# Kernel tuning notes

Measured on AMD Instinct MI355X. Metric: run time of the kernel, lower is better.

Reference implementation:

```python
import jax, jax.numpy as jnp
import numpy as np

# ---- model hyperparameters (match init_kwargs) ----
D_MODEL = 1024
D_STATE = 128
EXPAND = 2
HEADDIM = 64
NGROUPS = 1
D_INNER = EXPAND * D_MODEL            # 2048
NHEADS = D_INNER // HEADDIM           # 32
ROPE_FRAC = 0.5
SPLIT = int(D_STATE * ROPE_FRAC)      # 64 rotary dims
NANG = SPLIT // 2                     # 32 rope angles
A_FLOOR = 1e-4
EPS = 1e-5
BATCH, SEQLEN = 1, 1024
SIZES = [D_INNER, D_INNER, D_STATE * NGROUPS, D_STATE * NGROUPS, NHEADS, NHEADS, NHEADS, NANG]
D_IN_PROJ = int(np.sum(SIZES))        # 4480


def setup_inputs() -> dict:
    key = jax.random.key(0)
    ks = jax.random.split(key, 6)
    u = jax.random.normal(ks[0], (BATCH, SEQLEN, D_MODEL), dtype=jnp.float32)
    W_in = jax.random.normal(ks[1], (D_MODEL, D_IN_PROJ), dtype=jnp.float32) * 0.02
    # dt_bias ~ log(dt) for dt in [1e-3, 0.1] -> around -4
    dt_bias = jax.random.normal(ks[2], (NHEADS,), dtype=jnp.float32) * 0.5 - 4.0
    B_bias = jnp.ones((NHEADS, D_STATE), jnp.float32) + 0.01 * jax.random.normal(ks[3], (NHEADS, D_STATE), dtype=jnp.float32)
    C_bias = jnp.ones((NHEADS, D_STATE), jnp.float32) + 0.01 * jax.random.normal(ks[4], (NHEADS, D_STATE), dtype=jnp.float32)
    Bn_w = jnp.ones((D_STATE,), jnp.float32)
    Cn_w = jnp.ones((D_STATE,), jnp.float32)
    D_param = jnp.ones((NHEADS,), jnp.float32)
    W_out = jax.random.normal(ks[5], (D_INNER, D_MODEL), dtype=jnp.float32) * 0.02
    return {"u": u, "W_in": W_in, "dt_bias": dt_bias, "B_bias": B_bias, "C_bias": C_bias,
            "Bn_w": Bn_w, "Cn_w": Cn_w, "D_param": D_param, "W_out": W_out}


def _rmsnorm(v, w):
    return v * jax.lax.rsqrt(jnp.mean(v * v, axis=-1, keepdims=True) + EPS) * w


def _forward(u, W_in, dt_bias, B_bias, C_bias, Bn_w, Cn_w, D_param, W_out):
    b, l, _ = u.shape
    proj = u @ W_in                                   # (b, l, d_in_proj)
    idx = np.cumsum(SIZES)[:-1]
    z, x, Bp, Cp, dd_dt, dd_A, trap_raw, ang = jnp.split(proj, idx, axis=-1)
    z = z.reshape(b, l, NHEADS, HEADDIM)
    x = x.reshape(b, l, NHEADS, HEADDIM)
    # A = clamp(-softplus(.), max=-A_floor);  dt = softplus(. + dt_bias)
    A = jnp.minimum(-jax.nn.softplus(dd_A), -A_FLOOR)          # (b,l,H)
    dt = jax.nn.softplus(dd_dt + dt_bias)                      # (b,l,H)
    a = jnp.exp(A * dt)                                        # decay per step
    lam = jax.nn.sigmoid(trap_raw)                             # trapezoid gate
    # RMSNorm on B/C (ngroups=1), then per-head additive bias
    Bn = _rmsnorm(Bp, Bn_w)                                    # (b,l,N)
    Cn = _rmsnorm(Cp, Cn_w)
    Bh = Bn[:, :, None, :] + B_bias                            # (b,l,H,N)
    Ch = Cn[:, :, None, :] + C_bias
    # data-dependent rotary: cumulative angle = cumsum(angles * dt)
    theta = jnp.cumsum(ang[:, :, None, :] * dt[..., None], axis=1)  # (b,l,H,NANG)
    cos, sin = jnp.cos(theta), jnp.sin(theta)

    def rope(v):
        d1, d2, rest = v[..., :NANG], v[..., NANG:SPLIT], v[..., SPLIT:]
        return jnp.concatenate([d1 * cos - d2 * sin, d1 * sin + d2 * cos, rest], axis=-1)

    Bh, Ch = rope(Bh), rope(Ch)

    tfirst = lambda v: jnp.moveaxis(v, 1, 0)
    inputs = (tfirst(Bh), tfirst(Ch), tfirst(x), tfirst(a), tfirst(dt), tfirst(lam))
    h0 = jnp.zeros((b, NHEADS, HEADDIM, D_STATE), jnp.float32)
    k0 = jnp.zeros((b, NHEADS, D_STATE), jnp.float32)
    v0 = jnp.zeros((b, NHEADS, HEADDIM), jnp.float32)

    def step(carry, inp):
        h, kp, vp = carry
        Bt, Ct, xt, at, dtt, lamt = inp
        # trapezoidal selective-scan update:
        # h_t = a_t h_{t-1} + dt_t (lam_t B_t x_t + (1-lam_t) a_t B_{t-1} x_{t-1})
        cur = jnp.einsum('bhp,bhn->bhpn', xt, Bt) * (dtt * lamt)[..., None, None]
        prv = jnp.einsum('bhp,bhn->bhpn', vp, kp) * (dtt * (1.0 - lamt) * at)[..., None, None]
        h = at[..., None, None] * h + cur + prv
        yt = jnp.einsum('bhn,bhpn->bhp', Ct, h)
        return (h, Bt, xt), yt

    _, y = jax.lax.scan(step, (h0, k0, v0), inputs)          # (l,b,H,P)
    y = jnp.moveaxis(y, 0, 1) + D_param[None, None, :, None] * x
    y = y * jax.nn.silu(z)                                    # gated output (no out-proj norm)
    return y.reshape(b, l, D_INNER) @ W_out


def reference(u, W_in, dt_bias, B_bias, C_bias, Bn_w, Cn_w, D_param, W_out):
    return _forward(u, W_in, dt_bias, B_bias, C_bias, Bn_w, Cn_w, D_param, W_out)
```

## Files before the change

### kernel.cpp

```cpp
#include <hip/hip_runtime.h>
#include <stdint.h>

#define SEQ     1024

typedef __attribute__((ext_vector_type(8))) short short8;
typedef __attribute__((ext_vector_type(4))) float f4;

__device__ __forceinline__ short f2b(float f){
  union { float f; uint32_t u; } v; v.f = f;
  uint32_t r = (v.u + 0x7fffu + ((v.u >> 16) & 1u)) >> 16;
  return (short)(uint16_t)r;
}
__device__ __forceinline__ float b2f(uint16_t u){
  union { uint32_t u; float f; } v; v.u = ((uint32_t)u) << 16; return v.f;
}
__device__ __forceinline__ uint32_t pack2(float lo, float hi){
  return (uint32_t)(uint16_t)f2b(lo) | ((uint32_t)(uint16_t)f2b(hi) << 16);
}
__device__ __forceinline__ float softplus_f(float x){
  return x > 20.f ? x : log1pf(__expf(x));
}
__device__ __forceinline__ void gload_lds16(const short* g, short* l){
  __builtin_amdgcn_global_load_lds((const __attribute__((address_space(1))) void*)g,
                                   (__attribute__((address_space(3))) void*)l, 16, 0, 0);
}

__global__ __launch_bounds__(256) void prep_inputs(const float* __restrict__ u, short* __restrict__ u16,
                                                   const float* __restrict__ W_in, short* __restrict__ WtIn,
                                                   const float* __restrict__ W_out, short* __restrict__ WtOut,
                                                   float* __restrict__ outz){
  int b = blockIdx.x;
  int tid = threadIdx.x;
  if (b < 1024){
    int i = (b * 256 + tid) * 4;
    f4 v = *(const f4*)(u + i);
    uint2 pk; pk.x = pack2(v.x, v.y); pk.y = pack2(v.z, v.w);
    *(uint2*)(u16 + i) = pk;
    return;
  }
  if (b >= 2656){
    int i = ((b - 2656) * 256 + tid) * 4;
    *(f4*)(outz + i) = (f4){0.f, 0.f, 0.f, 0.f};
    return;
  }
  const float* in; short* outp; int R, lda, bx, by;
  if (b < 2144){ int idx = b - 1024; bx = idx % 140; by = idx / 140; in = W_in;  outp = WtIn;  R = 1024; lda = 4480; }
  else         { int idx = b - 2144; bx = idx & 31;  by = idx >> 5;  in = W_out; outp = WtOut; R = 2048; lda = 1024; }
  __shared__ float tile[32][132];
  int bc = bx * 32, br = by * 128;
  int c = tid & 31, r0 = tid >> 5;
  #pragma unroll
  for (int i = 0; i < 16; i++){
    int r = r0 + i * 8;
    tile[c][r] = in[(size_t)(br + r) * lda + bc + c];
  }
  __syncthreads();
  #pragma unroll
  for (int i = 0; i < 4; i++){
    int task = tid + 256 * i;
    int cc = task >> 5;
    int rg = (task & 31) * 4;
    f4 v = *(const f4*)&tile[cc][rg];
    uint2 pk; pk.x = pack2(v.x, v.y); pk.y = pack2(v.z, v.w);
    *(uint2*)(outp + (size_t)(bc + cc) * R + br + rg) = pk;
  }
}

__global__ __launch_bounds__(256) void gemm1_kernel(const short* __restrict__ A, const short* __restrict__ Bt,
                                                    short* __restrict__ zx, short* __restrict__ xTb,
                                                    float* __restrict__ projT){
  const int K = 1024;
  __shared__ __align__(16) short As[2][128 * 32];
  __shared__ __align__(16) short Bs[2][160 * 32];
  const int tid  = threadIdx.x;
  const int wave = tid >> 6;
  const int lane = tid & 63;
  const int m0 = blockIdx.y * 128;
  const int n0 = blockIdx.x * 160;
  const int wm = (wave >> 1) * 64;
  const int wn = (wave & 1) * 80;
  const int quad = lane >> 4;
  const int r16  = lane & 15;

  f4 acc[4][5];
  #pragma unroll
  for (int i = 0; i < 4; i++)
    #pragma unroll
    for (int j = 0; j < 5; j++) acc[i][j] = (f4){0.f, 0.f, 0.f, 0.f};

  const int row0 = tid >> 2;
  const int kq   = tid & 3;
  const short* gA0 = A  + (size_t)(m0 + row0) * K + kq * 8;
  const short* gA1 = A  + (size_t)(m0 + row0 + 64) * K + kq * 8;
  const short* gB0 = Bt + (size_t)(n0 + row0) * K + kq * 8;
  const short* gB1 = Bt + (size_t)(n0 + row0 + 64) * K + kq * 8;
  const short* gB2 = Bt + (size_t)(n0 + row0 + 128) * K + kq * 8;

  gload_lds16(gA0, &As[0][(size_t)tid * 8]);
  gload_lds16(gA1, &As[0][(size_t)(tid + 256) * 8]);
  gload_lds16(gB0, &Bs[0][(size_t)tid * 8]);
  gload_lds16(gB1, &Bs[0][(size_t)(tid + 256) * 8]);
  if (tid < 128) gload_lds16(gB2, &Bs[0][(size_t)(tid + 512) * 8]);

  for (int kt = 0; kt < 32; ++kt){
    const int cur = kt & 1;
    __syncthreads();
    if (kt + 1 < 32){
      const int ko = (kt + 1) * 32;
      const int nxt = cur ^ 1;
      gload_lds16(gA0 + ko, &As[nxt][(size_t)tid * 8]);
      gload_lds16(gA1 + ko, &As[nxt][(size_t)(tid + 256) * 8]);
      gload_lds16(gB0 + ko, &Bs[nxt][(size_t)tid * 8]);
      gload_lds16(gB1 + ko, &Bs[nxt][(size_t)(tid + 256) * 8]);
      if (tid < 128) gload_lds16(gB2 + ko, &Bs[nxt][(size_t)(tid + 512) * 8]);
    }
    short8 af[4], bf[5];
    #pragma unroll
    for (int i = 0; i < 4; i++)
      af[i] = *(const short8*)&As[cur][(wm + i * 16 + r16) * 32 + quad * 8];
    #pragma unroll
    for (int j = 0; j < 5; j++)
      bf[j] = *(const short8*)&Bs[cur][(wn + j * 16 + r16) * 32 + quad * 8];
    #pragma unroll
    for (int i = 0; i < 4; i++)
      #pragma unroll
      for (int j = 0; j < 5; j++)
        acc[i][j] = __builtin_amdgcn_mfma_f32_16x16x32_bf16(af[i], bf[j], acc[i][j], 0, 0, 0);
  }

  #pragma unroll
  for (int i = 0; i < 4; i++)
    #pragma unroll
    for (int j = 0; j < 5; j++){
      int colb = n0 + wn + j * 16 + r16;
      int rowb = m0 + wm + i * 16 + quad * 4;
      if (colb < 2048){
        #pragma unroll
        for (int rr = 0; rr < 4; ++rr)
          zx[(size_t)(rowb + rr) * 4096 + colb] = f2b(acc[i][j][rr]);
      } else if (colb < 4096){
        uint2 pk; pk.x = pack2(acc[i][j][0], acc[i][j][1]); pk.y = pack2(acc[i][j][2], acc[i][j][3]);
        *(uint2*)(xTb + (size_t)(colb - 2048) * 1024 + rowb) = pk;
        #pragma unroll
        for (int rr = 0; rr < 4; ++rr)
          zx[(size_t)(rowb + rr) * 4096 + colb] = f2b(acc[i][j][rr]);
      } else {
        #pragma unroll
        for (int rr = 0; rr < 4; ++rr)
          projT[(size_t)(rowb + rr) * 384 + (colb - 4096)] = acc[i][j][rr];
      }
    }
}

__global__ __launch_bounds__(256) void gemm2_kernel(const short* __restrict__ A, const short* __restrict__ Bt,
                                                    float* __restrict__ C){
  const int N = 1024, K = 2048, klen = 512;
  __shared__ __align__(16) short As[2][128 * 32];
  __shared__ __align__(16) short Bs[2][128 * 32];
  const int tid  = threadIdx.x;
  const int wave = tid >> 6;
  const int lane = tid & 63;
  const int m0 = blockIdx.y * 128;
  const int n0 = blockIdx.x * 128;
  const int k0 = blockIdx.z * klen;
  const int wm = (wave >> 1) * 64;
  const int wn = (wave & 1) * 64;
  const int quad = lane >> 4;
  const int r16  = lane & 15;

  f4 acc[4][4];
  #pragma unroll
  for (int i = 0; i < 4; i++)
    #pragma unroll
    for (int j = 0; j < 4; j++) acc[i][j] = (f4){0.f, 0.f, 0.f, 0.f};

  const int row0 = tid >> 2;
  const int kq   = tid & 3;
  const short* gA0 = A  + (size_t)(m0 + row0) * K + k0 + kq * 8;
  const short* gA1 = A  + (size_t)(m0 + row0 + 64) * K + k0 + kq * 8;
  const short* gB0 = Bt + (size_t)(n0 + row0) * K + k0 + kq * 8;
  const short* gB1 = Bt + (size_t)(n0 + row0 + 64) * K + k0 + kq * 8;

  gload_lds16(gA0, &As[0][(size_t)tid * 8]);
  gload_lds16(gA1, &As[0][(size_t)(tid + 256) * 8]);
  gload_lds16(gB0, &Bs[0][(size_t)tid * 8]);
  gload_lds16(gB1, &Bs[0][(size_t)(tid + 256) * 8]);

  for (int kt = 0; kt < klen / 32; ++kt){
    const int cur = kt & 1;
    __syncthreads();
    if (kt + 1 < klen / 32){
      const int ko = (kt + 1) * 32;
      const int nxt = cur ^ 1;
      gload_lds16(gA0 + ko, &As[nxt][(size_t)tid * 8]);
      gload_lds16(gA1 + ko, &As[nxt][(size_t)(tid + 256) * 8]);
      gload_lds16(gB0 + ko, &Bs[nxt][(size_t)tid * 8]);
      gload_lds16(gB1 + ko, &Bs[nxt][(size_t)(tid + 256) * 8]);
    }
    short8 af[4], bf[4];
    #pragma unroll
    for (int i = 0; i < 4; i++){
      af[i] = *(const short8*)&As[cur][(wm + i * 16 + r16) * 32 + quad * 8];
      bf[i] = *(const short8*)&Bs[cur][(wn + i * 16 + r16) * 32 + quad * 8];
    }
    #pragma unroll
    for (int i = 0; i < 4; i++)
      #pragma unroll
      for (int j = 0; j < 4; j++)
        acc[i][j] = __builtin_amdgcn_mfma_f32_16x16x32_bf16(af[i], bf[j], acc[i][j], 0, 0, 0);
  }

  #pragma unroll
  for (int i = 0; i < 4; i++)
    #pragma unroll
    for (int j = 0; j < 4; j++)
      #pragma unroll
      for (int rr = 0; rr < 4; ++rr){
        int row = m0 + wm + i * 16 + quad * 4 + rr;
        int col = n0 + wn + j * 16 + r16;
        unsafeAtomicAdd(&C[(size_t)row * N + col], acc[i][j][rr]);
      }
}

__global__ __launch_bounds__(256) void scan_theta(const float* __restrict__ projT,
                                                  const float* __restrict__ dt_bias,
                                                  float* __restrict__ Lcum, float* __restrict__ u2b,
                                                  float* __restrict__ c1b,
                                                  float* __restrict__ cosb, float* __restrict__ sinb){
  int b = blockIdx.x;
  int tid = threadIdx.x;
  int t0 = tid * 4;
  int lane = tid & 63, wave = tid >> 6;
  __shared__ float wsum[4];
  if (b < 32){
    int h = b;
    float dtbias = dt_bias[h];
    float dt5[5], lam5[5];
    #pragma unroll
    for (int i = 0; i < 5; i++){
      int t = t0 + i;
      if (t < 1024){
        const float* row = projT + (size_t)t * 384;
        dt5[i]  = softplus_f(row[256 + h] + dtbias);
        lam5[i] = 1.f / (1.f + __expf(-row[320 + h]));
      } else { dt5[i] = 0.f; lam5[i] = 0.f; }
    }
    float v[4], c1[4], c2n[4];
    #pragma unroll
    for (int i = 0; i < 4; i++){
      int t = t0 + i;
      const float* row = projT + (size_t)t * 384;
      float Ah = -fmaxf(softplus_f(row[288 + h]), 1e-4f);
      v[i]   = Ah * dt5[i];
      c1[i]  = dt5[i] * lam5[i];
      c2n[i] = dt5[i + 1] * (1.f - lam5[i + 1]);
    }
    v[1] += v[0]; v[2] += v[1]; v[3] += v[2];
    float tot = v[3], sc = tot;
    #pragma unroll
    for (int off = 1; off < 64; off <<= 1){
      float n = __shfl_up(sc, off, 64);
      if (lane >= off) sc += n;
    }
    if (lane == 63) wsum[wave] = sc;
    __syncthreads();
    float base = sc - tot;
    for (int w = 0; w < wave; ++w) base += wsum[w];
    #pragma unroll
    for (int i = 0; i < 4; i++){
      int t = t0 + i;
      Lcum[h * 1024 + t] = base + v[i];
      u2b[h * 1024 + t]  = c1[i] + c2n[i];
      c1b[h * 1024 + t]  = c1[i];
    }
  } else {
    int hk = b - 32;
    int h = hk >> 5, k = hk & 31;
    float dtbias = dt_bias[h];
    float v[4];
    #pragma unroll
    for (int i = 0; i < 4; i++){
      const float* row = projT + (size_t)(t0 + i) * 384;
      float dt = softplus_f(row[256 + h] + dtbias);
      v[i] = row[352 + k] * dt;
    }
    v[1] += v[0]; v[2] += v[1]; v[3] += v[2];
    float tot = v[3], sc = tot;
    #pragma unroll
    for (int off = 1; off < 64; off <<= 1){
      float n = __shfl_up(sc, off, 64);
      if (lane >= off) sc += n;
    }
    if (lane == 63) wsum[wave] = sc;
    __syncthreads();
    float base = sc - tot;
    for (int w = 0; w < wave; ++w) base += wsum[w];
    #pragma unroll
    for (int i = 0; i < 4; i++){
      float th = base + v[i];
      float s, c;
      __sincosf(th, &s, &c);
      int t = t0 + i;
      cosb[(size_t)t * 1024 + h * 32 + k] = c;
      sinb[(size_t)t * 1024 + h * 32 + k] = s;
    }
  }
}

__global__ __launch_bounds__(256) void bcxt_kernel(const float* __restrict__ projT,
                                                   const float* __restrict__ B_bias, const float* __restrict__ C_bias,
                                                   const float* __restrict__ Bn_w, const float* __restrict__ Cn_w,
                                                   const float* __restrict__ cosb, const float* __restrict__ sinb,
                                                   short* __restrict__ Bb, short* __restrict__ Cb){
  int t = blockIdx.x;
  int tid = threadIdx.x;
  __shared__ float vv[2][128];
  __shared__ float red[4];
  int n = tid & 127;
  int isC = tid >> 7;
  float val = projT[(size_t)t * 384 + isC * 128 + n];
  float ss = val * val;
  #pragma unroll
  for (int off = 32; off >= 1; off >>= 1) ss += __shfl_down(ss, off);
  int wave = tid >> 6, lane = tid & 63;
  if (lane == 0) red[wave] = ss;
  __syncthreads();
  float rsv = isC ? rsqrtf((red[2] + red[3]) * (1.f / 128.f) + 1e-5f)
                  : rsqrtf((red[0] + red[1]) * (1.f / 128.f) + 1e-5f);
  vv[isC][n] = val * rsv * (isC ? Cn_w[n] : Bn_w[n]);
  __syncthreads();
  const float* cb = cosb + (size_t)t * 1024;
  const float* sb = sinb + (size_t)t * 1024;
  #pragma unroll
  for (int it = 0; it < 8; it++){
    int task = tid + 256 * it;
    int arr  = task >> 10;
    int rem  = task & 1023;
    int h    = rem >> 5;
    int n0   = (rem & 31) * 4;
    const float* bias = arr ? C_bias : B_bias;
    const float* base = vv[arr];
    f4 bv = *(const f4*)&base[n0];
    f4 bi = *(const f4*)&bias[h * 128 + n0];
    f4 o;
    if (n0 < 32){
      f4 bv2 = *(const f4*)&base[n0 + 32];
      f4 bi2 = *(const f4*)&bias[h * 128 + n0 + 32];
      f4 cv = *(const f4*)&cb[h * 32 + n0];
      f4 sv = *(const f4*)&sb[h * 32 + n0];
      #pragma unroll
      for (int q = 0; q < 4; q++) o[q] = (bv[q] + bi[q]) * cv[q] - (bv2[q] + bi2[q]) * sv[q];
    } else if (n0 < 64){
      int k0 = n0 - 32;
      f4 bv1 = *(const f4*)&base[k0];
      f4 bi1 = *(const f4*)&bias[h * 128 + k0];
      f4 cv = *(const f4*)&cb[h * 32 + k0];
      f4 sv = *(const f4*)&sb[h * 32 + k0];
      #pragma unroll
      for (int q = 0; q < 4; q++) o[q] = (bv1[q] + bi1[q]) * sv[q] + (bv[q] + bi[q]) * cv[q];
    } else {
      #pragma unroll
      for (int q = 0; q < 4; q++) o[q] = bv[q] + bi[q];
    }
    uint2 pk; pk.x = pack2(o.x, o.y); pk.y = pack2(o.z, o.w);
    short* outp = arr ? Cb : Bb;
    *(uint2*)(outp + (size_t)t * 4096 + h * 128 + n0) = pk;
  }
}

__global__ __launch_bounds__(256) void hpart_kernel(const short* __restrict__ xTb, const short* __restrict__ Bb,
                                                    const float* __restrict__ Lcum, const float* __restrict__ u2b,
                                                    short* __restrict__ Hpart){
  int h = blockIdx.x >> 4, c = (blockIdx.x >> 1) & 7, nh = blockIdx.x & 1;
  int t0 = c * 128;
  int tid = threadIdx.x;
  __shared__ float wS[128];
  if (tid < 128){
    float Lend = Lcum[h * 1024 + t0 + 127];
    wS[tid] = __expf(Lend - Lcum[h * 1024 + t0 + tid]) * u2b[h * 1024 + t0 + tid];
  }
  __syncthreads();
  int wave = tid >> 6, lane = tid & 63, quad = lane >> 4, r16 = lane & 15;
  int n0 = nh * 64 + wave * 16;
  f4 acc[4];
  #pragma unroll
  for (int i = 0; i < 4; i++) acc[i] = (f4){0.f, 0.f, 0.f, 0.f};

  const ushort* Bh = (const ushort*)Bb + (size_t)t0 * 4096 + h * 128;
  #pragma unroll
  for (int kk = 0; kk < 4; ++kk){
    int sb = kk * 32 + quad * 8;
    short8 af[4];
    #pragma unroll
    for (int i = 0; i < 4; i++){
      int p = i * 16 + r16;
      af[i] = *(const short8*)(xTb + (size_t)(h * 64 + p) * 1024 + t0 + sb);
    }
    float wv[8];
    #pragma unroll
    for (int jj = 0; jj < 8; jj++) wv[jj] = wS[sb + jj];
    int nn = n0 + r16;
    float e[8];
    #pragma unroll
    for (int jj = 0; jj < 8; jj++)
      e[jj] = b2f(Bh[(size_t)(sb + jj) * 4096 + nn]) * wv[jj];
    union { short8 s; uint32_t u[4]; } fr;
    #pragma unroll
    for (int q = 0; q < 4; q++) fr.u[q] = pack2(e[2 * q], e[2 * q + 1]);
    short8 bfr = fr.s;
    #pragma unroll
    for (int i = 0; i < 4; i++)
      acc[i] = __builtin_amdgcn_mfma_f32_16x16x32_bf16(af[i], bfr, acc[i], 0, 0, 0);
  }

  short* out = Hpart + ((size_t)(h * 8 + c)) * 8192;
  int nn = n0 + r16;
  #pragma unroll
  for (int i = 0; i < 4; i++)
    #pragma unroll
    for (int rr = 0; rr < 4; ++rr){
      int p = i * 16 + quad * 4 + rr;
      out[p * 128 + nn] = f2b(acc[i][rr]);
    }
}

#define GS 144
__global__ __launch_bounds__(256) void chunky_kernel(const short* __restrict__ Cb, const short* __restrict__ Bbg,
                                                     const short* __restrict__ xTb, const short* __restrict__ Hpart,
                                                     const float* __restrict__ Lcum, const float* __restrict__ u2b,
                                                     const float* __restrict__ c1b,
                                                     const short* __restrict__ zx, const float* __restrict__ D_par,
                                                     short* __restrict__ yb16){
  int h = blockIdx.x >> 4, c = (blockIdx.x >> 1) & 7, half = blockIdx.x & 1;
  int t0 = c * 128;
  int tb = half * 64;
  __shared__ __align__(16) short Gt[64 * GS];
  __shared__ __align__(16) short Hu[64 * 128];
  __shared__ float Lc[128], u2v[128], c1v[128];
  int tid = threadIdx.x;
  if (tid < 128){
    Lc[tid]  = Lcum[h * 1024 + t0 + tid];
    u2v[tid] = u2b[h * 1024 + t0 + tid];
    c1v[tid] = c1b[h * 1024 + t0 + tid];
  }
  float Lprev = (c > 0) ? Lcum[h * 1024 + t0 - 1] : 0.f;
  float Dp = D_par[h];

  {
    float hacc[32];
    #pragma unroll
    for (int q = 0; q < 32; q++) hacc[q] = 0.f;
    for (int cp = 0; cp < c; ++cp){
      float dec = __expf(Lprev - Lcum[h * 1024 + cp * 128 + 127]);
      const short8* hp = (const short8*)((const ushort*)Hpart + ((size_t)(h * 8 + cp)) * 8192 + tid * 32);
      #pragma unroll
      for (int q = 0; q < 4; q++){
        short8 v = hp[q];
        #pragma unroll
        for (int e = 0; e < 8; e++) hacc[q * 8 + e] += dec * b2f((uint16_t)v[e]);
      }
    }
    int p = tid >> 2;
    int wbase = tid * 64;
    #pragma unroll
    for (int q = 0; q < 4; q++){
      union { short8 s; uint32_t u[4]; } fr;
      #pragma unroll
      for (int p2 = 0; p2 < 4; p2++) fr.u[p2] = pack2(hacc[q * 8 + p2 * 2], hacc[q * 8 + p2 * 2 + 1]);
      int off = (wbase + q * 16) ^ ((p & 7) << 4);
      *(short8*)((char*)Hu + off) = fr.s;
    }
  }

  int wave = tid >> 6, lane = tid & 63, quad = lane >> 4, r16 = lane & 15;
  int wm2 = (wave >> 1) * 32, wn2 = (wave & 1) * 64;

  f4 acc[2][4];
  #pragma unroll
  for (int i = 0; i < 2; i++)
    #pragma unroll
    for (int j = 0; j < 4; j++) acc[i][j] = (f4){0.f, 0.f, 0.f, 0.f};
  #pragma unroll
  for (int kk = 0; kk < 4; ++kk){
    short8 af[2], bf[4];
    #pragma unroll
    for (int i = 0; i < 2; i++)
      af[i] = *(const short8*)(Cb + (size_t)(t0 + tb + wm2 + i * 16 + r16) * 4096 + h * 128 + kk * 32 + quad * 8);
    #pragma unroll
    for (int j = 0; j < 4; j++)
      bf[j] = *(const short8*)(Bbg + (size_t)(t0 + wn2 + j * 16 + r16) * 4096 + h * 128 + kk * 32 + quad * 8);
    #pragma unroll
    for (int i = 0; i < 2; i++)
      #pragma unroll
      for (int j = 0; j < 4; j++)
        acc[i][j] = __builtin_amdgcn_mfma_f32_16x16x32_bf16(af[i], bf[j], acc[i][j], 0, 0, 0);
  }
  __syncthreads();

  #pragma unroll
  for (int i = 0; i < 2; i++){
    #pragma unroll
    for (int rr = 0; rr < 4; ++rr){
      int tl = wm2 + i * 16 + quad * 4 + rr;
      int trow = tb + tl;
      float Lt = Lc[trow];
      #pragma unroll
      for (int j = 0; j < 4; j++){
        int scol = wn2 + j * 16 + r16;
        float g = 0.f;
        if (scol <= trow){
          float wcoef = (scol == trow) ? c1v[scol] : u2v[scol];
          g = acc[i][j][rr] * wcoef * __expf(Lt - Lc[scol]);
        }
        Gt[tl * GS + scol] = f2b(g);
      }
    }
  }
  __syncthreads();

  f4 accY[4], accZ[4];
  #pragma unroll
  for (int j = 0; j < 4; j++){ accY[j] = (f4){0.f,0.f,0.f,0.f}; accZ[j] = (f4){0.f,0.f,0.f,0.f}; }
  int m0 = wave * 16;
  #pragma unroll
  for (int kk = 0; kk < 4; ++kk){
    short8 ag, ac, bx[4], bh[4];
    ag = *(const short8*)&Gt[(m0 + r16) * GS + kk * 32 + quad * 8];
    ac = *(const short8*)(Cb + (size_t)(t0 + tb + m0 + r16) * 4096 + h * 128 + kk * 32 + quad * 8);
    #pragma unroll
    for (int j = 0; j < 4; j++){
      bx[j] = *(const short8*)(xTb + (size_t)(h * 64 + j * 16 + r16) * 1024 + t0 + kk * 32 + quad * 8);
      int hrow = j * 16 + r16;
      int hoff = (hrow * 256 + kk * 64 + quad * 16) ^ ((hrow & 7) << 4);
      bh[j] = *(const short8*)((const char*)Hu + hoff);
    }
    #pragma unroll
    for (int j = 0; j < 4; j++){
      accY[j] = __builtin_amdgcn_mfma_f32_16x16x32_bf16(ag, bx[j], accY[j], 0, 0, 0);
      accZ[j] = __builtin_amdgcn_mfma_f32_16x16x32_bf16(ac, bh[j], accZ[j], 0, 0, 0);
    }
  }
  const ushort* zxu = (const ushort*)zx;
  #pragma unroll
  for (int rr = 0; rr < 4; ++rr){
    int tl = m0 + quad * 4 + rr;
    int trow = tb + tl;
    float ei = __expf(Lc[trow] - Lprev);
    const ushort* zrow = zxu + (size_t)(t0 + trow) * 4096;
    #pragma unroll
    for (int j = 0; j < 4; j++){
      int col = h * 64 + j * 16 + r16;
      float zv = b2f(zrow[col]);
      float xv = b2f(zrow[2048 + col]);
      float yv = accY[j][rr] + ei * accZ[j][rr] + Dp * xv;
      float o = yv * (zv / (1.f + __expf(-zv)));
      yb16[(size_t)(t0 + trow) * 2048 + col] = f2b(o);
    }
  }
}

extern "C" void kernel_launch(void* const* d_in, const int* in_sizes, int n_in,
                              void* d_out, int out_size, void* d_ws, size_t ws_size,
                              hipStream_t stream){
  const float* u       = (const float*)d_in[0];
  const float* W_in    = (const float*)d_in[1];
  const float* dt_bias = (const float*)d_in[2];
  const float* B_bias  = (const float*)d_in[3];
  const float* C_bias  = (const float*)d_in[4];
  const float* Bn_w    = (const float*)d_in[5];
  const float* Cn_w    = (const float*)d_in[6];
  const float* D_par   = (const float*)d_in[7];
  const float* W_out   = (const float*)d_in[8];
  float* out = (float*)d_out;

  char* ws = (char*)d_ws;
  short* u16   = (short*)(ws + 0);
  short* WtIn  = (short*)(ws + 2097152);
  short* WtOut = (short*)(ws + 11272192);
  short* zx    = (short*)(ws + 15466496);
  float* projT = (float*)(ws + 23855104);
  float* cosb  = (float*)(ws + 25427968);
  float* sinb  = (float*)(ws + 29622272);
  short* Bb    = (short*)(ws + 33816576);
  short* Cb    = (short*)(ws + 42205184);
  short* xTb   = (short*)(ws + 50593792);
  float* Lcum  = (float*)(ws + 54788096);
  float* u2b   = (float*)(ws + 54919168);
  float* c1b   = (float*)(ws + 55050240);
  short* Hpart = (short*)(ws + 55181312);
  short* yb16  = (short*)(ws + 59375616);

  prep_inputs<<<3680, 256, 0, stream>>>(u, u16, W_in, WtIn, W_out, WtOut, out);
  gemm1_kernel<<<dim3(28, 8), 256, 0, stream>>>(u16, WtIn, zx, xTb, projT);
  scan_theta<<<1056, 256, 0, stream>>>(projT, dt_bias, Lcum, u2b, c1b, cosb, sinb);
  bcxt_kernel<<<1024, 256, 0, stream>>>(projT, B_bias, C_bias, Bn_w, Cn_w, cosb, sinb, Bb, Cb);
  hpart_kernel<<<512, 256, 0, stream>>>(xTb, Bb, Lcum, u2b, Hpart);
  chunky_kernel<<<512, 256, 0, stream>>>(Cb, Bb, xTb, Hpart, Lcum, u2b, c1b, zx, D_par, yb16);
  gemm2_kernel<<<dim3(8, 8, 4), 256, 0, stream>>>(yb16, WtOut, out);
}
```

Before: 203.7 us.

## Deepen GEMM K-tiles to 64 with XOR-swizzled LDS and retile out-projection

Both GEMMs now stage 64-wide K tiles in LDS instead of 32, halving the number of barrier-separated iterations. Rows are written with an XOR swizzle on 16-byte chunks to avoid LDS bank conflicts on the MFMA fragment reads. The output-projection GEMM switches to 64x128 tiles with a split-K of 2 instead of 128x128 with split-K of 4, which halves the atomic adds into the output. The cost is double the LDS per block, which may lower occupancy.

```diff
diff --git a/kernel.cpp b/kernel.cpp
--- a/kernel.cpp
+++ b/kernel.cpp
@@ -70,8 +70,8 @@
                                                     short* __restrict__ zx, short* __restrict__ xTb,
                                                     float* __restrict__ projT){
   const int K = 1024;
-  __shared__ __align__(16) short As[2][128 * 32];
-  __shared__ __align__(16) short Bs[2][160 * 32];
+  __shared__ __align__(16) short As[2][128 * 64];
+  __shared__ __align__(16) short Bs[2][160 * 64];
   const int tid  = threadIdx.x;
   const int wave = tid >> 6;
   const int lane = tid & 63;
@@ -81,6 +81,7 @@
   const int wn = (wave & 1) * 80;
   const int quad = lane >> 4;
   const int r16  = lane & 15;
+  const int rsw  = r16 & 7;
 
   f4 acc[4][5];
   #pragma unroll
@@ -88,44 +89,44 @@
     #pragma unroll
     for (int j = 0; j < 5; j++) acc[i][j] = (f4){0.f, 0.f, 0.f, 0.f};
 
-  const int row0 = tid >> 2;
-  const int kq   = tid & 3;
-  const short* gA0 = A  + (size_t)(m0 + row0) * K + kq * 8;
-  const short* gA1 = A  + (size_t)(m0 + row0 + 64) * K + kq * 8;
-  const short* gB0 = Bt + (size_t)(n0 + row0) * K + kq * 8;
-  const short* gB1 = Bt + (size_t)(n0 + row0 + 64) * K + kq * 8;
-  const short* gB2 = Bt + (size_t)(n0 + row0 + 128) * K + kq * 8;
-
-  gload_lds16(gA0, &As[0][(size_t)tid * 8]);
-  gload_lds16(gA1, &As[0][(size_t)(tid + 256) * 8]);
-  gload_lds16(gB0, &Bs[0][(size_t)tid * 8]);
-  gload_lds16(gB1, &Bs[0][(size_t)(tid + 256) * 8]);
-  if (tid < 128) gload_lds16(gB2, &Bs[0][(size_t)(tid + 512) * 8]);
-
-  for (int kt = 0; kt < 32; ++kt){
+  const int srow = tid >> 3;
+  const int soct = tid & 7;
+  const int og   = (soct ^ (srow & 7)) * 8;
+  const short* gA0 = A  + (size_t)(m0 + srow) * K + og;
+  const short* gB0 = Bt + (size_t)(n0 + srow) * K + og;
+
+  #pragma unroll
+  for (int i = 0; i < 4; i++) gload_lds16(gA0 + (size_t)i * 32 * K, &As[0][tid * 8 + i * 2048]);
+  #pragma unroll
+  for (int i = 0; i < 5; i++) gload_lds16(gB0 + (size_t)i * 32 * K, &Bs[0][tid * 8 + i * 2048]);
+
+  for (int kt = 0; kt < 16; ++kt){
     const int cur = kt & 1;
     __syncthreads();
-    if (kt + 1 < 32){
-      const int ko = (kt + 1) * 32;
+    if (kt + 1 < 16){
+      const int ko = (kt + 1) * 64;
       const int nxt = cur ^ 1;
-      gload_lds16(gA0 + ko, &As[nxt][(size_t)tid * 8]);
-      gload_lds16(gA1 + ko, &As[nxt][(size_t)(tid + 256) * 8]);
-      gload_lds16(gB0 + ko, &Bs[nxt][(size_t)tid * 8]);
-      gload_lds16(gB1 + ko, &Bs[nxt][(size_t)(tid + 256) * 8]);
-      if (tid < 128) gload_lds16(gB2 + ko, &Bs[nxt][(size_t)(tid + 512) * 8]);
-    }
-    short8 af[4], bf[5];
-    #pragma unroll
-    for (int i = 0; i < 4; i++)
-      af[i] = *(const short8*)&As[cur][(wm + i * 16 + r16) * 32 + quad * 8];
-    #pragma unroll
-    for (int j = 0; j < 5; j++)
-      bf[j] = *(const short8*)&Bs[cur][(wn + j * 16 + r16) * 32 + quad * 8];
-    #pragma unroll
-    for (int i = 0; i < 4; i++)
+      #pragma unroll
+      for (int i = 0; i < 4; i++) gload_lds16(gA0 + (size_t)i * 32 * K + ko, &As[nxt][tid * 8 + i * 2048]);
+      #pragma unroll
+      for (int i = 0; i < 5; i++) gload_lds16(gB0 + (size_t)i * 32 * K + ko, &Bs[nxt][tid * 8 + i * 2048]);
+    }
+    #pragma unroll
+    for (int ks = 0; ks < 2; ++ks){
+      const int oq = ((ks * 4 + quad) ^ rsw) * 8;
+      short8 af[4], bf[5];
+      #pragma unroll
+      for (int i = 0; i < 4; i++)
+        af[i] = *(const short8*)&As[cur][(wm + i * 16 + r16) * 64 + oq];
       #pragma unroll
       for (int j = 0; j < 5; j++)
-        acc[i][j] = __builtin_amdgcn_mfma_f32_16x16x32_bf16(af[i], bf[j], acc[i][j], 0, 0, 0);
+        bf[j] = *(const short8*)&Bs[cur][(wn + j * 16 + r16) * 64 + oq];
+      #pragma unroll
+      for (int i = 0; i < 4; i++)
+        #pragma unroll
+        for (int j = 0; j < 5; j++)
+          acc[i][j] = __builtin_amdgcn_mfma_f32_16x16x32_bf16(af[i], bf[j], acc[i][j], 0, 0, 0);
+    }
   }
 
   #pragma unroll
@@ -154,64 +155,69 @@
 
 __global__ __launch_bounds__(256) void gemm2_kernel(const short* __restrict__ A, const short* __restrict__ Bt,
                                                     float* __restrict__ C){
-  const int N = 1024, K = 2048, klen = 512;
-  __shared__ __align__(16) short As[2][128 * 32];
-  __shared__ __align__(16) short Bs[2][128 * 32];
+  const int N = 1024, K = 2048, klen = 1024;
+  __shared__ __align__(16) short As[2][64 * 64];
+  __shared__ __align__(16) short Bs[2][128 * 64];
   const int tid  = threadIdx.x;
   const int wave = tid >> 6;
   const int lane = tid & 63;
-  const int m0 = blockIdx.y * 128;
+  const int m0 = blockIdx.y * 64;
   const int n0 = blockIdx.x * 128;
   const int k0 = blockIdx.z * klen;
-  const int wm = (wave >> 1) * 64;
+  const int wm = (wave >> 1) * 32;
   const int wn = (wave & 1) * 64;
   const int quad = lane >> 4;
   const int r16  = lane & 15;
-
-  f4 acc[4][4];
-  #pragma unroll
-  for (int i = 0; i < 4; i++)
+  const int rsw  = r16 & 7;
+
+  f4 acc[2][4];
+  #pragma unroll
+  for (int i = 0; i < 2; i++)
     #pragma unroll
     for (int j = 0; j < 4; j++) acc[i][j] = (f4){0.f, 0.f, 0.f, 0.f};
 
-  const int row0 = tid >> 2;
-  const int kq   = tid & 3;
-  const short* gA0 = A  + (size_t)(m0 + row0) * K + k0 + kq * 8;
-  const short* gA1 = A  + (size_t)(m0 + row0 + 64) * K + k0 + kq * 8;
-  const short* gB0 = Bt + (size_t)(n0 + row0) * K + k0 + kq * 8;
-  const short* gB1 = Bt + (size_t)(n0 + row0 + 64) * K + k0 + kq * 8;
-
-  gload_lds16(gA0, &As[0][(size_t)tid * 8]);
-  gload_lds16(gA1, &As[0][(size_t)(tid + 256) * 8]);
-  gload_lds16(gB0, &Bs[0][(size_t)tid * 8]);
-  gload_lds16(gB1, &Bs[0][(size_t)(tid + 256) * 8]);
-
-  for (int kt = 0; kt < klen / 32; ++kt){
+  const int srow = tid >> 3;
+  const int soct = tid & 7;
+  const int og   = (soct ^ (srow & 7)) * 8;
+  const short* gA0 = A  + (size_t)(m0 + srow) * K + k0 + og;
+  const short* gB0 = Bt + (size_t)(n0 + srow) * K + k0 + og;
+
+  #pragma unroll
+  for (int i = 0; i < 2; i++) gload_lds16(gA0 + (size_t)i * 32 * K, &As[0][tid * 8 + i * 2048]);
+  #pragma unroll
+  for (int i = 0; i < 4; i++) gload_lds16(gB0 + (size_t)i * 32 * K, &Bs[0][tid * 8 + i * 2048]);
+
+  for (int kt = 0; kt < 16; ++kt){
     const int cur = kt & 1;
     __syncthreads();
-    if (kt + 1 < klen / 32){
-      const int ko = (kt + 1) * 32;
+    if (kt + 1 < 16){
+      const int ko = (kt + 1) * 64;
       const int nxt = cur ^ 1;
-      gload_lds16(gA0 + ko, &As[nxt][(size_t)tid * 8]);
-      gload_lds16(gA1 + ko, &As[nxt][(size_t)(tid + 256) * 8]);
-      gload_lds16(gB0 + ko, &Bs[nxt][(size_t)tid * 8]);
-      gload_lds16(gB1 + ko, &Bs[nxt][(size_t)(tid + 256) * 8]);
-    }
-    short8 af[4], bf[4];
-    #pragma unroll
-    for (int i = 0; i < 4; i++){
-      af[i] = *(const short8*)&As[cur][(wm + i * 16 + r16) * 32 + quad * 8];
-      bf[i] = *(const short8*)&Bs[cur][(wn + i * 16 + r16) * 32 + quad * 8];
-    }
-    #pragma unroll
-    for (int i = 0; i < 4; i++)
+      #pragma unroll
+      for (int i = 0; i < 2; i++) gload_lds16(gA0 + (size_t)i * 32 * K + ko, &As[nxt][tid * 8 + i * 2048]);
+      #pragma unroll
+      for (int i = 0; i < 4; i++) gload_lds16(gB0 + (size_t)i * 32 * K + ko, &Bs[nxt][tid * 8 + i * 2048]);
+    }
+    #pragma unroll
+    for (int ks = 0; ks < 2; ++ks){
+      const int oq = ((ks * 4 + quad) ^ rsw) * 8;
+      short8 af[2], bf[4];
+      #pragma unroll
+      for (int i = 0; i < 2; i++)
+        af[i] = *(const short8*)&As[cur][(wm + i * 16 + r16) * 64 + oq];
       #pragma unroll
       for (int j = 0; j < 4; j++)
-        acc[i][j] = __builtin_amdgcn_mfma_f32_16x16x32_bf16(af[i], bf[j], acc[i][j], 0, 0, 0);
-  }
-
-  #pragma unroll
-  for (int i = 0; i < 4; i++)
+        bf[j] = *(const short8*)&Bs[cur][(wn + j * 16 + r16) * 64 + oq];
+      #pragma unroll
+      for (int i = 0; i < 2; i++)
+        #pragma unroll
+        for (int j = 0; j < 4; j++)
+          acc[i][j] = __builtin_amdgcn_mfma_f32_16x16x32_bf16(af[i], bf[j], acc[i][j], 0, 0, 0);
+    }
+  }
+
+  #pragma unroll
+  for (int i = 0; i < 2; i++)
     #pragma unroll
     for (int j = 0; j < 4; j++)
       #pragma unroll
@@ -596,5 +602,5 @@
   bcxt_kernel<<<1024, 256, 0, stream>>>(projT, B_bias, C_bias, Bn_w, Cn_w, cosb, sinb, Bb, Cb);
   hpart_kernel<<<512, 256, 0, stream>>>(xTb, Bb, Lcum, u2b, Hpart);
   chunky_kernel<<<512, 256, 0, stream>>>(Cb, Bb, xTb, Hpart, Lcum, u2b, c1b, zx, D_par, yb16);
-  gemm2_kernel<<<dim3(8, 8, 4), 256, 0, stream>>>(yb16, WtOut, out);
-}
+  gemm2_kernel<<<dim3(8, 16, 2), 256, 0, stream>>>(yb16, WtOut, out);
+}
```

Result: slower. 211.4 us (+3.8%).
